# Optimization experiments

Measured on AMD Instinct MI355X. Metric: run time of the kernel, lower is better.

Reference implementation:

```python
import jax, jax.numpy as jnp
import numpy as np

B, H, S, D = 2, 16, 2048, 128

def setup_inputs() -> dict:
    key = jax.random.key(0)
    kq, kk, kv = jax.random.split(key, 3)
    Q = jax.random.normal(kq, (B, H, S, D), dtype=jnp.float32)
    K = jax.random.normal(kk, (B, H, S, D), dtype=jnp.float32)
    V = jax.random.normal(kv, (B, H, S, D), dtype=jnp.float32)
    return {"Q": Q, "K": K, "V": V}

def reference(Q, K, V):
    # FlashAttentionV3 forward: scaled dot-product attention with causal mask,
    # scale defaults to 1/sqrt(head_dim), dropout=0.
    head_dim = Q.shape[-1]
    scale = 1.0 / jnp.sqrt(jnp.asarray(head_dim, dtype=Q.dtype))
    # scores: [B, H, S, S]
    scores = jnp.einsum('bhqd,bhkd->bhqk', Q, K) * scale
    seq_q, seq_k = Q.shape[2], K.shape[2]
    causal_mask = jnp.tril(jnp.ones((seq_q, seq_k), dtype=bool))  # [S, S]
    scores = jnp.where(causal_mask, scores, jnp.asarray(-jnp.inf, dtype=scores.dtype))
    attn = jax.nn.softmax(scores, axis=-1)
    out = jnp.einsum('bhqk,bhkd->bhqd', attn, V)
    return out
```

## Files before the change

### kernel.cpp

```cpp
#include <hip/hip_runtime.h>
#include <hip/hip_bf16.h>

typedef __attribute__((ext_vector_type(8))) short short8;
typedef __attribute__((ext_vector_type(4))) float f32x4;
typedef __attribute__((ext_vector_type(4))) unsigned int u32x4;

#define S_LEN 2048
#define D_DIM 128
#define NT 32
#define NQT 32
#define TILE_FRAG_BYTES 16384u
#define VF_OFF ((size_t)32 * NT * TILE_FRAG_BYTES)

__device__ __forceinline__ unsigned short bfbits(float f) {
  return __builtin_bit_cast(unsigned short, __float2bfloat16(f));
}
__device__ __forceinline__ unsigned int pk2(float lo, float hi) {
  return (unsigned int)bfbits(lo) | ((unsigned int)bfbits(hi) << 16);
}
__device__ __forceinline__ float exp2f_hw(float x) {
  float r;
  asm("v_exp_f32 %0, %1" : "=v"(r) : "v"(x));
  return r;
}
__device__ __forceinline__ void gload16(const void* g, void* l) {
  __builtin_amdgcn_global_load_lds(
      (const __attribute__((address_space(1))) unsigned int*)g,
      (__attribute__((address_space(3))) unsigned int*)l, 16, 0, 0);
}

extern "C" __global__ void __launch_bounds__(256)
fa_prepass_kernel(const float* __restrict__ Kg, const float* __restrict__ Vg,
                  char* __restrict__ ws)
{
  const unsigned gid = blockIdx.x * 256 + threadIdx.x;
  const unsigned g = gid & ((1u << 20) - 1);
  const int ln = g & 63, l15 = ln & 15, lhi = (ln >> 4) & 3;
  const int f  = (g >> 6) & 15;
  const int t  = (g >> 10) & 31;
  const int bh = g >> 15;
  char* dst = ws + ((size_t)(bh * NT + t) * 16 + f) * 1024 + ln * 16;
  if (gid < (1u << 20)) {
    const int c = f >> 2, kk = f & 3;
    const int row = t * 64 + ((l15 >> 2) << 3) + (l15 & 3) + ((c & 1) << 2) + ((c >> 1) << 5);
    const float* src = Kg + (size_t)bh * S_LEN * D_DIM + (size_t)row * D_DIM + kk * 32 + lhi * 8;
    f32x4 a = *(const f32x4*)src;
    f32x4 b = *(const f32x4*)(src + 4);
    u32x4 u;
    u[0] = pk2(a[0], a[1]); u[1] = pk2(a[2], a[3]);
    u[2] = pk2(b[0], b[1]); u[3] = pk2(b[2], b[3]);
    *(u32x4*)dst = u;
  } else {
    const int dc = f >> 1, w = f & 1;
    const float* src = Vg + (size_t)bh * S_LEN * D_DIM
                     + (size_t)(t * 64 + w * 32 + lhi * 8) * D_DIM + dc * 16 + l15;
    float v[8];
    #pragma unroll
    for (int j = 0; j < 8; ++j) v[j] = src[(size_t)j * D_DIM];
    u32x4 u;
    u[0] = pk2(v[0], v[1]); u[1] = pk2(v[2], v[3]);
    u[2] = pk2(v[4], v[5]); u[3] = pk2(v[6], v[7]);
    *(u32x4*)(dst + VF_OFF) = u;
  }
}

extern "C" __global__ void __launch_bounds__(128, 2)
fa_fwd_kernel(const float* __restrict__ Qg, const char* __restrict__ ws,
              float* __restrict__ Og)
{
  __shared__ __align__(16) char smem[2][16384];

  const int bh = blockIdx.x;
  const int by = (int)blockIdx.y;
  int qt;
  if      (by <  8) qt = 31 - by;
  else if (by < 16) qt = by - 8;
  else if (by < 24) qt = 39 - by;
  else              qt = by - 16;
  const int tid = threadIdx.x;
  const int wv  = tid >> 6;
  const int ln  = tid & 63;
  const int l15 = ln & 15;
  const int lhi = ln >> 4;

  const float* Qb = Qg + (size_t)bh * S_LEN * D_DIM;
  float*       Ob = Og + (size_t)bh * S_LEN * D_DIM;
  const char*  kfb = ws + (size_t)bh * NT * TILE_FRAG_BYTES;
  const char*  vfbg = kfb + VF_OFF;
  const int    voff = ln * 16;

  const float scale = 0.12753102f;
  const int wrow_lo = qt * 64 + wv * 32;

  short8 qf[2][4];
  #pragma unroll
  for (int g = 0; g < 2; ++g) {
    const float* qsrc = Qb + (size_t)(wrow_lo + g * 16 + l15) * D_DIM + lhi * 8;
    #pragma unroll
    for (int kk = 0; kk < 4; ++kk) {
      f32x4 a = *(const f32x4*)(qsrc + kk * 32);
      f32x4 b = *(const f32x4*)(qsrc + kk * 32 + 4);
      u32x4 u;
      u[0] = pk2(a[0] * scale, a[1] * scale);
      u[1] = pk2(a[2] * scale, a[3] * scale);
      u[2] = pk2(b[0] * scale, b[1] * scale);
      u[3] = pk2(b[2] * scale, b[3] * scale);
      qf[g][kk] = __builtin_bit_cast(short8, u);
    }
  }

  auto stage_k = [&](int t, char* buf) {
    const char* kt = kfb + (size_t)t * TILE_FRAG_BYTES;
    #pragma unroll
    for (int i = 0; i < 8; ++i) {
      const int fi = wv * 8 + i;
      gload16(kt + (size_t)fi * 1024 + voff, buf + fi * 1024);
    }
  };

  const f32x4 fzero = {0.f, 0.f, 0.f, 0.f};
  f32x4 oacc[2][8];
  #pragma unroll
  for (int g = 0; g < 2; ++g)
    #pragma unroll
    for (int i = 0; i < 8; ++i) oacc[g][i] = fzero;
  float m_run[2] = {8.0f, 8.0f};
  float l_run[2] = {0.f, 0.f};

  const int ntiles = qt + 1;

  stage_k(0, smem[0]);
  __syncthreads();

  int cur = 0;
  for (int t = 0; t < ntiles; ++t) {
    if (t + 1 < ntiles) stage_k(t + 1, smem[cur ^ 1]);

    const char* vg = vfbg + (size_t)t * TILE_FRAG_BYTES;
    short8 vf[16];
    #pragma unroll
    for (int i = 0; i < 16; ++i)
      vf[i] = *(const short8*)(vg + i * 1024 + voff);

    const char* kt = smem[cur];

    f32x4 sacc[2][4];
    __builtin_amdgcn_s_setprio(1);
    #pragma unroll
    for (int c = 0; c < 4; ++c) {
      sacc[0][c] = fzero; sacc[1][c] = fzero;
      #pragma unroll
      for (int kk = 0; kk < 4; ++kk) {
        short8 kf = *(const short8*)(kt + (c * 4 + kk) * 1024 + voff);
        sacc[0][c] = __builtin_amdgcn_mfma_f32_16x16x32_bf16(kf, qf[0][kk], sacc[0][c], 0, 0, 0);
        sacc[1][c] = __builtin_amdgcn_mfma_f32_16x16x32_bf16(kf, qf[1][kk], sacc[1][c], 0, 0, 0);
      }
    }
    __builtin_amdgcn_s_setprio(0);

    if (t == ntiles - 1) {
      #pragma unroll
      for (int g = 0; g < 2; ++g) {
        const int qg = wrow_lo + g * 16 + l15;
        #pragma unroll
        for (int c = 0; c < 4; ++c) {
          const int kvb = t * 64 + (c >> 1) * 32 + (c & 1) * 4 + lhi * 8;
          #pragma unroll
          for (int r = 0; r < 4; ++r)
            if (kvb + r > qg) sacc[g][c][r] = -INFINITY;
        }
      }
    }

    float mt[2];
    #pragma unroll
    for (int g = 0; g < 2; ++g) {
      float mA[4];
      #pragma unroll
      for (int r = 0; r < 4; ++r)
        mA[r] = fmaxf(fmaxf(sacc[g][0][r], sacc[g][1][r]),
                      fmaxf(sacc[g][2][r], sacc[g][3][r]));
      mt[g] = fmaxf(fmaxf(mA[0], mA[1]), fmaxf(mA[2], mA[3]));
      #pragma unroll
      for (int c = 0; c < 4; ++c)
        #pragma unroll
        for (int r = 0; r < 4; ++r)
          sacc[g][c][r] = exp2f_hw(sacc[g][c][r] - m_run[g]);
    }
    #pragma unroll
    for (int g = 0; g < 2; ++g) {
      float m = fmaxf(mt[g], __shfl_xor(mt[g], 16));
      m = fmaxf(m, __shfl_xor(m, 32));
      if (!__all(m <= m_run[g] + 11.5f)) {
        const float m_new = fmaxf(m_run[g], m);
        const float al = exp2f_hw(m_run[g] - m_new);
        #pragma unroll
        for (int c = 0; c < 4; ++c)
          #pragma unroll
          for (int r = 0; r < 4; ++r) sacc[g][c][r] *= al;
        #pragma unroll
        for (int dc = 0; dc < 8; ++dc)
          #pragma unroll
          for (int r = 0; r < 4; ++r) oacc[g][dc][r] *= al;
        l_run[g] *= al;
        m_run[g] = m_new;
      }
      float sA[4];
      #pragma unroll
      for (int r = 0; r < 4; ++r)
        sA[r] = (sacc[g][0][r] + sacc[g][1][r]) + (sacc[g][2][r] + sacc[g][3][r]);
      float rs = (sA[0] + sA[1]) + (sA[2] + sA[3]);
      rs += __shfl_xor(rs, 16);
      rs += __shfl_xor(rs, 32);
      l_run[g] += rs;
    }

    short8 pfrag[2][2];
    #pragma unroll
    for (int g = 0; g < 2; ++g)
      #pragma unroll
      for (int w = 0; w < 2; ++w) {
        u32x4 u;
        u[0] = pk2(sacc[g][2 * w][0], sacc[g][2 * w][1]);
        u[1] = pk2(sacc[g][2 * w][2], sacc[g][2 * w][3]);
        u[2] = pk2(sacc[g][2 * w + 1][0], sacc[g][2 * w + 1][1]);
        u[3] = pk2(sacc[g][2 * w + 1][2], sacc[g][2 * w + 1][3]);
        pfrag[g][w] = __builtin_bit_cast(short8, u);
      }

    __builtin_amdgcn_s_setprio(1);
    #pragma unroll
    for (int dc = 0; dc < 8; ++dc)
      #pragma unroll
      for (int w = 0; w < 2; ++w) {
        oacc[0][dc] = __builtin_amdgcn_mfma_f32_16x16x32_bf16(vf[dc * 2 + w], pfrag[0][w], oacc[0][dc], 0, 0, 0);
        oacc[1][dc] = __builtin_amdgcn_mfma_f32_16x16x32_bf16(vf[dc * 2 + w], pfrag[1][w], oacc[1][dc], 0, 0, 0);
      }
    __builtin_amdgcn_s_setprio(0);

    __syncthreads();
    cur ^= 1;
  }

  #pragma unroll
  for (int g = 0; g < 2; ++g) {
    const float invl = 1.0f / l_run[g];
    float* orow = Ob + (size_t)(wrow_lo + g * 16 + l15) * D_DIM + lhi * 4;
    #pragma unroll
    for (int dc = 0; dc < 8; ++dc) {
      f32x4 o;
      #pragma unroll
      for (int r = 0; r < 4; ++r) o[r] = oacc[g][dc][r] * invl;
      *(f32x4*)(orow + dc * 16) = o;
    }
  }
}

extern "C" void kernel_launch(void* const* d_in, const int* in_sizes, int n_in,
                              void* d_out, int out_size, void* d_ws, size_t ws_size,
                              hipStream_t stream) {
  const float* Q = (const float*)d_in[0];
  const float* K = (const float*)d_in[1];
  const float* V = (const float*)d_in[2];
  float* O = (float*)d_out;
  char* ws = (char*)d_ws;
  fa_prepass_kernel<<<dim3(8192), dim3(256), 0, stream>>>(K, V, ws);
  dim3 grid(32 , NQT);
  fa_fwd_kernel<<<grid, dim3(128), 0, stream>>>(Q, ws, O);
}
```

Measured before the change: 87.03 us.

## Software-pipeline PV MFMA one tile behind QK and defer softmax row-sum reduction

The P·V MFMAs for tile t-1 now run right after the Q·K^T MFMAs of tile t, so the exp, pack and V-fragment load work for the current tile can overlap with matrix work. The max-driven rescale moves to after that delayed PV step and uses the previous tile's max. The row sum is kept as a per-lane partial and reduced across lanes with shuffles only once at the end, which removes per-tile cross-lane traffic. In exchange, each tile's exponentials are taken against a running max that does not yet include that tile's scores. That weakens overflow and precision safety for inputs with large score jumps, and it keeps the V and P fragments live across iterations, raising register pressure.

```diff
diff --git a/kernel.cpp b/kernel.cpp
--- a/kernel.cpp
+++ b/kernel.cpp
@@ -125,7 +125,11 @@
     #pragma unroll
     for (int i = 0; i < 8; ++i) oacc[g][i] = fzero;
   float m_run[2] = {8.0f, 8.0f};
-  float l_run[2] = {0.f, 0.f};
+  float l_part[2] = {0.f, 0.f};
+  float mtp[2];
+
+  short8 vf[16];
+  short8 pf[2][2];
 
   const int ntiles = qt + 1;
 
@@ -136,14 +140,7 @@
   for (int t = 0; t < ntiles; ++t) {
     if (t + 1 < ntiles) stage_k(t + 1, smem[cur ^ 1]);
 
-    const char* vg = vfbg + (size_t)t * TILE_FRAG_BYTES;
-    short8 vf[16];
-    #pragma unroll
-    for (int i = 0; i < 16; ++i)
-      vf[i] = *(const short8*)(vg + i * 1024 + voff);
-
     const char* kt = smem[cur];
-
     f32x4 sacc[2][4];
     __builtin_amdgcn_s_setprio(1);
     #pragma unroll
@@ -157,6 +154,39 @@
       }
     }
     __builtin_amdgcn_s_setprio(0);
+
+    if (t > 0) {
+      __builtin_amdgcn_s_setprio(1);
+      #pragma unroll
+      for (int dc = 0; dc < 8; ++dc)
+        #pragma unroll
+        for (int w = 0; w < 2; ++w) {
+          oacc[0][dc] = __builtin_amdgcn_mfma_f32_16x16x32_bf16(vf[dc * 2 + w], pf[0][w], oacc[0][dc], 0, 0, 0);
+          oacc[1][dc] = __builtin_amdgcn_mfma_f32_16x16x32_bf16(vf[dc * 2 + w], pf[1][w], oacc[1][dc], 0, 0, 0);
+        }
+      __builtin_amdgcn_s_setprio(0);
+
+      #pragma unroll
+      for (int g = 0; g < 2; ++g) {
+        if (!__all(mtp[g] <= m_run[g] + 11.5f)) {
+          float m = fmaxf(mtp[g], __shfl_xor(mtp[g], 16));
+          m = fmaxf(m, __shfl_xor(m, 32));
+          const float m_new = fmaxf(m_run[g], m);
+          const float al = exp2f_hw(m_run[g] - m_new);
+          #pragma unroll
+          for (int dc = 0; dc < 8; ++dc)
+            #pragma unroll
+            for (int r = 0; r < 4; ++r) oacc[g][dc][r] *= al;
+          l_part[g] *= al;
+          m_run[g] = m_new;
+        }
+      }
+    }
+
+    const char* vg = vfbg + (size_t)t * TILE_FRAG_BYTES;
+    #pragma unroll
+    for (int i = 0; i < 16; ++i)
+      vf[i] = *(const short8*)(vg + i * 1024 + voff);
 
     if (t == ntiles - 1) {
       #pragma unroll
@@ -172,7 +202,6 @@
       }
     }
 
-    float mt[2];
     #pragma unroll
     for (int g = 0; g < 2; ++g) {
       float mA[4];
@@ -180,44 +209,20 @@
       for (int r = 0; r < 4; ++r)
         mA[r] = fmaxf(fmaxf(sacc[g][0][r], sacc[g][1][r]),
                       fmaxf(sacc[g][2][r], sacc[g][3][r]));
-      mt[g] = fmaxf(fmaxf(mA[0], mA[1]), fmaxf(mA[2], mA[3]));
+      mtp[g] = fmaxf(fmaxf(mA[0], mA[1]), fmaxf(mA[2], mA[3]));
+
       #pragma unroll
       for (int c = 0; c < 4; ++c)
         #pragma unroll
         for (int r = 0; r < 4; ++r)
           sacc[g][c][r] = exp2f_hw(sacc[g][c][r] - m_run[g]);
-    }
-    #pragma unroll
-    for (int g = 0; g < 2; ++g) {
-      float m = fmaxf(mt[g], __shfl_xor(mt[g], 16));
-      m = fmaxf(m, __shfl_xor(m, 32));
-      if (!__all(m <= m_run[g] + 11.5f)) {
-        const float m_new = fmaxf(m_run[g], m);
-        const float al = exp2f_hw(m_run[g] - m_new);
-        #pragma unroll
-        for (int c = 0; c < 4; ++c)
-          #pragma unroll
-          for (int r = 0; r < 4; ++r) sacc[g][c][r] *= al;
-        #pragma unroll
-        for (int dc = 0; dc < 8; ++dc)
-          #pragma unroll
-          for (int r = 0; r < 4; ++r) oacc[g][dc][r] *= al;
-        l_run[g] *= al;
-        m_run[g] = m_new;
-      }
+
       float sA[4];
       #pragma unroll
       for (int r = 0; r < 4; ++r)
         sA[r] = (sacc[g][0][r] + sacc[g][1][r]) + (sacc[g][2][r] + sacc[g][3][r]);
-      float rs = (sA[0] + sA[1]) + (sA[2] + sA[3]);
-      rs += __shfl_xor(rs, 16);
-      rs += __shfl_xor(rs, 32);
-      l_run[g] += rs;
-    }
-
-    short8 pfrag[2][2];
-    #pragma unroll
-    for (int g = 0; g < 2; ++g)
+      l_part[g] += (sA[0] + sA[1]) + (sA[2] + sA[3]);
+
       #pragma unroll
       for (int w = 0; w < 2; ++w) {
         u32x4 u;
@@ -225,26 +230,30 @@
         u[1] = pk2(sacc[g][2 * w][2], sacc[g][2 * w][3]);
         u[2] = pk2(sacc[g][2 * w + 1][0], sacc[g][2 * w + 1][1]);
         u[3] = pk2(sacc[g][2 * w + 1][2], sacc[g][2 * w + 1][3]);
-        pfrag[g][w] = __builtin_bit_cast(short8, u);
-      }
-
-    __builtin_amdgcn_s_setprio(1);
-    #pragma unroll
-    for (int dc = 0; dc < 8; ++dc)
-      #pragma unroll
-      for (int w = 0; w < 2; ++w) {
-        oacc[0][dc] = __builtin_amdgcn_mfma_f32_16x16x32_bf16(vf[dc * 2 + w], pfrag[0][w], oacc[0][dc], 0, 0, 0);
-        oacc[1][dc] = __builtin_amdgcn_mfma_f32_16x16x32_bf16(vf[dc * 2 + w], pfrag[1][w], oacc[1][dc], 0, 0, 0);
-      }
-    __builtin_amdgcn_s_setprio(0);
+        pf[g][w] = __builtin_bit_cast(short8, u);
+      }
+    }
 
     __syncthreads();
     cur ^= 1;
   }
 
+  __builtin_amdgcn_s_setprio(1);
+  #pragma unroll
+  for (int dc = 0; dc < 8; ++dc)
+    #pragma unroll
+    for (int w = 0; w < 2; ++w) {
+      oacc[0][dc] = __builtin_amdgcn_mfma_f32_16x16x32_bf16(vf[dc * 2 + w], pf[0][w], oacc[0][dc], 0, 0, 0);
+      oacc[1][dc] = __builtin_amdgcn_mfma_f32_16x16x32_bf16(vf[dc * 2 + w], pf[1][w], oacc[1][dc], 0, 0, 0);
+    }
+  __builtin_amdgcn_s_setprio(0);
+
   #pragma unroll
   for (int g = 0; g < 2; ++g) {
-    const float invl = 1.0f / l_run[g];
+    float l = l_part[g];
+    l += __shfl_xor(l, 16);
+    l += __shfl_xor(l, 32);
+    const float invl = 1.0f / l;
     float* orow = Ob + (size_t)(wrow_lo + g * 16 + l15) * D_DIM + lhi * 4;
     #pragma unroll
     for (int dc = 0; dc < 8; ++dc) {
```

After: 81.49 us. 6.4% less time.
